# Kernel optimization log

Measured on AMD Instinct MI355X. Metric: run time of the kernel, lower is better.

## Reference

```python
import jax, jax.numpy as jnp
import numpy as np

SCALE_MIN, SCALE_MAX = 0.01, 10.0
LN_EPS = 1e-5

B, KIN, H, C = 32, 6144, 512, 5


def _kaiming_uniform(k, shape):
    # torch kaiming_uniform_(a=sqrt(5)) on (out,in): bound = 1/sqrt(fan_in)
    bound = 1.0 / np.sqrt(shape[1])
    return jax.random.uniform(k, shape, minval=-bound, maxval=bound, dtype=jnp.float32)


def setup_inputs() -> dict:
    key = jax.random.key(0)
    ks = jax.random.split(key, 16)
    inp = {"x": jax.random.normal(ks[0], (B, KIN), dtype=jnp.float32)}
    dims = [(H, KIN), (H, H), (H, H)]
    for i, (o, n) in enumerate(dims):
        inp[f"w{i}"] = _kaiming_uniform(ks[1 + 3 * i], (o, n))
        inp[f"t{i}"] = jax.random.uniform(ks[2 + 3 * i], (o, n), minval=-1.0, maxval=1.0, dtype=jnp.float32)
        inp[f"s{i}"] = jax.random.uniform(ks[3 + 3 * i], (o, n), minval=-2.0, maxval=0.0, dtype=jnp.float32)
        inp[f"g{i}"] = jnp.ones((o,), jnp.float32)
        inp[f"b{i}"] = jnp.zeros((o,), jnp.float32)
    inp["cw"] = _kaiming_uniform(ks[10], (C, H))
    cbound = 1.0 / np.sqrt(H)
    inp["cb"] = jax.random.uniform(ks[11], (C,), minval=-cbound, maxval=cbound, dtype=jnp.float32)
    return inp


def _wavelet_linear(h, w, t, sr):
    # h: (B, in), params: (out, in)
    scale = SCALE_MIN + (SCALE_MAX - SCALE_MIN) * jax.nn.sigmoid(sr)
    s = (h[:, None, :] - t[None]) / (scale[None] + 1e-8)  # (B, out, in)
    psi = (1.0 - s * s) * jnp.exp(-0.5 * s * s)  # mexican hat
    return jnp.einsum('boi,oi->bo', psi, w)


def _layer_norm(h, g, b):
    m = jnp.mean(h, axis=-1, keepdims=True)
    v = jnp.mean(jnp.square(h - m), axis=-1, keepdims=True)
    return (h - m) * jax.lax.rsqrt(v + LN_EPS) * g + b


def reference(x, w0, t0, s0, g0, b0, w1, t1, s1, g1, b1, w2, t2, s2, g2, b2, cw, cb):
    h = x
    for (w, t, sr, g, b) in [(w0, t0, s0, g0, b0), (w1, t1, s1, g1, b1), (w2, t2, s2, g2, b2)]:
        h = _layer_norm(jax.nn.silu(_wavelet_linear(h, w, t, sr)), g, b)
    return h @ cw.T + cb
```

## Files before the change

### kernel.cpp

```cpp
#include <hip/hip_runtime.h>

#define LN_EPS 1e-5f
#define LOG2E 1.44269504f
#define NHALF_LOG2E (-0.72134752f)

#if __has_builtin(__builtin_amdgcn_exp2f)
#define EXP2F(x) __builtin_amdgcn_exp2f(x)
#else
#define EXP2F(x) __expf((x) * 0.69314718f)
#endif


constexpr int NBLK   = 512;
constexpr int TPB    = 512;
constexpr int NWAVES = NBLK * (TPB / 64);
constexpr int NGRP   = 16;
constexpr int GRP    = NBLK / NGRP;
constexpr int PADX   = 34;

__device__ __forceinline__ float sysld(const float* p)
{
    return __hip_atomic_load(p, __ATOMIC_RELAXED, __HIP_MEMORY_SCOPE_SYSTEM);
}
__device__ __forceinline__ void sysst(float* p, float v)
{
    __hip_atomic_store(p, v, __ATOMIC_RELAXED, __HIP_MEMORY_SCOPE_SYSTEM);
}
__device__ __forceinline__ float2 sysld2(const float* p)
{
    unsigned long long v = __hip_atomic_load((const unsigned long long*)p,
        __ATOMIC_RELAXED, __HIP_MEMORY_SCOPE_SYSTEM);
    union { unsigned long long u; float2 f; } c; c.u = v; return c.f;
}
__device__ __forceinline__ void sysst2(float* p, float a, float b)
{
    union { unsigned long long u; float2 f; } c; c.f = make_float2(a, b);
    __hip_atomic_store((unsigned long long*)p, c.u, __ATOMIC_RELAXED,
                       __HIP_MEMORY_SCOPE_SYSTEM);
}

__device__ __forceinline__ void gridbar(int* __restrict__ bar, int k)
{
    asm volatile("s_waitcnt vmcnt(0)" ::: "memory");
    __syncthreads();
    if (threadIdx.x == 0) {
        const int g = blockIdx.x >> 5;
        int* grpArr = bar + g * 32;
        int* grpRel = bar + (NGRP + g) * 32;
        int* gArr   = bar + 2 * NGRP * 32;

        int old = __hip_atomic_fetch_add(grpArr, 1, __ATOMIC_RELAXED,
                                         __HIP_MEMORY_SCOPE_AGENT);
        if (old == k * GRP - 1) {
            int o2 = __hip_atomic_fetch_add(gArr, 1, __ATOMIC_RELAXED,
                                            __HIP_MEMORY_SCOPE_AGENT);
            if (o2 == k * NGRP - 1) {
#pragma unroll
                for (int j = 0; j < NGRP; ++j)
                    __hip_atomic_store(bar + (NGRP + j) * 32, k,
                                       __ATOMIC_RELAXED, __HIP_MEMORY_SCOPE_AGENT);
            }
        }
        while (__hip_atomic_load(grpRel, __ATOMIC_RELAXED,
                                 __HIP_MEMORY_SCOPE_AGENT) < k)
            __builtin_amdgcn_s_sleep(8);
    }
    __syncthreads();
}

__device__ __forceinline__ void wav0_phase(const float* __restrict__ x,
        const float* __restrict__ w, const float* __restrict__ t,
        const float* __restrict__ s, float* __restrict__ part,
        float4* __restrict__ myPrep, float* __restrict__ xs,
        int lane, int wave)
{
    constexpr int RANGE = 192, STEPS = RANGE / 4, TPW = 4;
    const int si    = blockIdx.x >> 4;
    const int obase = (blockIdx.x & 15) * 32;
    const int ibase = si * RANGE;

    for (int b = wave; b < 32; b += 8)
        for (int i2 = lane; i2 < RANGE; i2 += 64)
            xs[i2 * PADX + b] = x[b * 6144 + ibase + i2];
    __syncthreads();

    const int p = lane & 15, g = lane >> 4;
    const int o0 = obase + wave * TPW;
    const float* __restrict__ wp = w + (size_t)o0 * 6144 + ibase;
    const float* __restrict__ tp = t + (size_t)o0 * 6144 + ibase;
    const float* __restrict__ sp = s + (size_t)o0 * 6144 + ibase;

    float fw[3], ft[3], fs[3];
#pragma unroll
    for (int r = 0; r < 3; ++r) {
        int il = r * 64 + lane;
        fw[r] = wp[il]; ft[r] = tp[il]; fs[r] = sp[il];
    }

#pragma unroll
    for (int ti = 0; ti < TPW; ++ti) {
#pragma unroll
        for (int r = 0; r < 3; ++r) {
            int il = r * 64 + lane;
            float sig = __builtin_amdgcn_rcpf(1.f + EXP2F(-fs[r] * LOG2E));
            float inv = __builtin_amdgcn_rcpf(fmaf(9.99f, sig, 0.01000001f));
            myPrep[il] = make_float4(inv, -ft[r] * inv, fw[r], 0.f);
        }
        if (ti + 1 < TPW) {
            const float* wpn = wp + (size_t)(ti + 1) * 6144;
            const float* tpn = tp + (size_t)(ti + 1) * 6144;
            const float* spn = sp + (size_t)(ti + 1) * 6144;
#pragma unroll
            for (int r = 0; r < 3; ++r) {
                int il = r * 64 + lane;
                fw[r] = wpn[il]; ft[r] = tpn[il]; fs[r] = spn[il];
            }
        }

        float acc0 = 0.f, acc1 = 0.f;
#pragma unroll 8
        for (int st = 0; st < STEPS; ++st) {
            float4 pr = myPrep[st * 4 + g];
            float2 xv = *(const float2*)&xs[(st * 4 + g) * PADX + 2 * p];
            float u0 = fmaf(xv.x, pr.x, pr.y);
            float u1 = fmaf(xv.y, pr.x, pr.y);
            float q0 = u0 * u0, q1 = u1 * u1;
            float e0 = EXP2F(q0 * NHALF_LOG2E);
            float e1 = EXP2F(q1 * NHALF_LOG2E);
            float pw0 = fmaf(-pr.z, q0, pr.z);
            float pw1 = fmaf(-pr.z, q1, pr.z);
            acc0 = fmaf(pw0, e0, acc0);
            acc1 = fmaf(pw1, e1, acc1);
        }

        acc0 += __shfl_down(acc0, 32); acc0 += __shfl_down(acc0, 16);
        acc1 += __shfl_down(acc1, 32); acc1 += __shfl_down(acc1, 16);
        if (lane < 16) {
            const int o = o0 + ti;
            sysst2(part + (size_t)si * 16384 + o * 32 + 2 * p, acc0, acc1);
        }
    }
}

__device__ __forceinline__ void wav12_phase(const float* __restrict__ hin,
        float* __restrict__ part, float4* __restrict__ myPrep,
        int lane, int gw, float fw, float ft, float fs)
{
    constexpr int STEPS = 16;
    const int p = lane & 15, g = lane >> 4;
    const int o = gw & 511, si = gw >> 9;
    const int ibase = si * 64;

    {
        float sig = __builtin_amdgcn_rcpf(1.f + EXP2F(-fs * LOG2E));
        float inv = __builtin_amdgcn_rcpf(fmaf(9.99f, sig, 0.01000001f));
        myPrep[lane] = make_float4(inv, -ft * inv, fw, 0.f);
    }

    const float* __restrict__ hp = hin + (size_t)(ibase + g) * 32 + 2 * p;

    float acc0 = 0.f, acc1 = 0.f;
#pragma unroll 8
    for (int st = 0; st < STEPS; ++st) {
        float4 pr = myPrep[st * 4 + g];
        float2 xv = sysld2(hp + (size_t)st * 128);
        float u0 = fmaf(xv.x, pr.x, pr.y);
        float u1 = fmaf(xv.y, pr.x, pr.y);
        float q0 = u0 * u0, q1 = u1 * u1;
        float e0 = EXP2F(q0 * NHALF_LOG2E);
        float e1 = EXP2F(q1 * NHALF_LOG2E);
        float pw0 = fmaf(-pr.z, q0, pr.z);
        float pw1 = fmaf(-pr.z, q1, pr.z);
        acc0 = fmaf(pw0, e0, acc0);
        acc1 = fmaf(pw1, e1, acc1);
    }

    acc0 += __shfl_down(acc0, 32); acc0 += __shfl_down(acc0, 16);
    acc1 += __shfl_down(acc1, 32); acc1 += __shfl_down(acc1, 16);
    if (lane < 16)
        sysst2(part + (size_t)si * 16384 + o * 32 + 2 * p, acc0, acc1);
}

template<int S>
__device__ __forceinline__ void ln_phase(const float* __restrict__ part,
        const float* __restrict__ gam, const float* __restrict__ bet,
        float* __restrict__ hT, float* __restrict__ r1, float* __restrict__ r2)
{
    if (blockIdx.x < 32) {
        const int b = blockIdx.x, tid = threadIdx.x;
        float v = 0.f;
#pragma unroll
        for (int si = 0; si < S; ++si)
            v += sysld(part + (size_t)si * 16384 + tid * 32 + b);
        float a = v * __builtin_amdgcn_rcpf(1.f + EXP2F(-v * LOG2E));

        float s1 = a, s2 = a * a;
#pragma unroll
        for (int off = 32; off; off >>= 1) {
            s1 += __shfl_down(s1, off);
            s2 += __shfl_down(s2, off);
        }
        const int lane = tid & 63, wid = tid >> 6;
        if (lane == 0) { r1[wid] = s1; r2[wid] = s2; }
        __syncthreads();
        float t1 = 0.f, t2 = 0.f;
#pragma unroll
        for (int k = 0; k < 8; ++k) { t1 += r1[k]; t2 += r2[k]; }
        float m   = t1 * (1.f / 512.f);
        float var = t2 * (1.f / 512.f) - m * m;
        float r   = __builtin_amdgcn_rsqf(var + LN_EPS);
        sysst(hT + tid * 32 + b, (a - m) * r * gam[tid] + bet[tid]);
    }
}

template<int S>
__device__ __forceinline__ void cls_phase(const float* __restrict__ part,
        const float* __restrict__ gam, const float* __restrict__ bet,
        const float* __restrict__ cw, const float* __restrict__ cb,
        float* __restrict__ out, float* __restrict__ r1, float* __restrict__ r2,
        float (* __restrict__ cr)[8])
{
    if (blockIdx.x < 32) {
        const int b = blockIdx.x, tid = threadIdx.x;
        float v = 0.f;
#pragma unroll
        for (int si = 0; si < S; ++si)
            v += sysld(part + (size_t)si * 16384 + tid * 32 + b);
        float a = v * __builtin_amdgcn_rcpf(1.f + EXP2F(-v * LOG2E));

        float s1 = a, s2 = a * a;
#pragma unroll
        for (int off = 32; off; off >>= 1) {
            s1 += __shfl_down(s1, off);
            s2 += __shfl_down(s2, off);
        }
        const int lane = tid & 63, wid = tid >> 6;
        if (lane == 0) { r1[wid] = s1; r2[wid] = s2; }
        __syncthreads();
        float t1 = 0.f, t2 = 0.f;
#pragma unroll
        for (int k = 0; k < 8; ++k) { t1 += r1[k]; t2 += r2[k]; }
        float m   = t1 * (1.f / 512.f);
        float var = t2 * (1.f / 512.f) - m * m;
        float r   = __builtin_amdgcn_rsqf(var + LN_EPS);
        float hl  = (a - m) * r * gam[tid] + bet[tid];

#pragma unroll
        for (int c = 0; c < 5; ++c) {
            float pv = hl * cw[c * 512 + tid];
#pragma unroll
            for (int off = 32; off; off >>= 1) pv += __shfl_down(pv, off);
            if (lane == 0) cr[c][wid] = pv;
        }
        __syncthreads();
        if (tid < 5) {
            float sum = 0.f;
#pragma unroll
            for (int k = 0; k < 8; ++k) sum += cr[tid][k];
            out[b * 5 + tid] = sum + cb[tid];
        }
    }
}

__global__ __launch_bounds__(TPB, 4)
void megakernel(const float* __restrict__ x,
                const float* __restrict__ w0, const float* __restrict__ t0,
                const float* __restrict__ s0, const float* __restrict__ g0,
                const float* __restrict__ b0,
                const float* __restrict__ w1, const float* __restrict__ t1,
                const float* __restrict__ s1, const float* __restrict__ g1,
                const float* __restrict__ b1,
                const float* __restrict__ w2, const float* __restrict__ t2,
                const float* __restrict__ s2, const float* __restrict__ g2,
                const float* __restrict__ b2,
                const float* __restrict__ cw, const float* __restrict__ cb,
                float* __restrict__ out,
                float* __restrict__ part, float* __restrict__ hT,
                int* __restrict__ bar)
{
    __shared__ float4 prep[8][192];
    __shared__ float  xs[192 * PADX];
    __shared__ float  r1[8], r2[8], cr[5][8];

    const int wave = threadIdx.x >> 6, lane = threadIdx.x & 63;
    const int gw = blockIdx.x * (TPB / 64) + wave;
    float4* myPrep = prep[wave];

    wav0_phase(x, w0, t0, s0, part, myPrep, xs, lane, wave);
    const int o1 = gw & 511, si1 = gw >> 9;
    const size_t off1 = (size_t)o1 * 512 + si1 * 64 + lane;
    float fw1 = w1[off1], ft1 = t1[off1], fs1 = s1[off1];
    gridbar(bar, 1);
    ln_phase<32>(part, g0, b0, hT, r1, r2);
    gridbar(bar, 2);

    wav12_phase(hT, part, myPrep, lane, gw, fw1, ft1, fs1);
    float fw2 = w2[off1], ft2 = t2[off1], fs2 = s2[off1];
    gridbar(bar, 3);
    ln_phase<8>(part, g1, b1, hT, r1, r2);
    gridbar(bar, 4);

    wav12_phase(hT, part, myPrep, lane, gw, fw2, ft2, fs2);
    gridbar(bar, 5);
    cls_phase<8>(part, g2, b2, cw, cb, out, r1, r2, cr);
}

extern "C" void kernel_launch(void* const* d_in, const int* in_sizes, int n_in,
                              void* d_out, int out_size, void* d_ws, size_t ws_size,
                              hipStream_t stream)
{
    const float* x  = (const float*)d_in[0];
    const float* w0 = (const float*)d_in[1];
    const float* t0 = (const float*)d_in[2];
    const float* s0 = (const float*)d_in[3];
    const float* g0 = (const float*)d_in[4];
    const float* b0 = (const float*)d_in[5];
    const float* w1 = (const float*)d_in[6];
    const float* t1 = (const float*)d_in[7];
    const float* s1 = (const float*)d_in[8];
    const float* g1 = (const float*)d_in[9];
    const float* b1 = (const float*)d_in[10];
    const float* w2 = (const float*)d_in[11];
    const float* t2 = (const float*)d_in[12];
    const float* s2 = (const float*)d_in[13];
    const float* g2 = (const float*)d_in[14];
    const float* b2 = (const float*)d_in[15];
    const float* cw = (const float*)d_in[16];
    const float* cb = (const float*)d_in[17];
    float* out = (float*)d_out;

    float* part = (float*)d_ws;
    float* hT   = part + 32 * 16384;
    int*   bar  = (int*)(hT + 16384);

    hipMemsetAsync(bar, 0, 8192, stream);

    void* args[] = { (void*)&x,
                     (void*)&w0, (void*)&t0, (void*)&s0, (void*)&g0, (void*)&b0,
                     (void*)&w1, (void*)&t1, (void*)&s1, (void*)&g1, (void*)&b1,
                     (void*)&w2, (void*)&t2, (void*)&s2, (void*)&g2, (void*)&b2,
                     (void*)&cw, (void*)&cb, (void*)&out,
                     (void*)&part, (void*)&hT, (void*)&bar };

    hipLaunchKernel((const void*)megakernel, dim3(NBLK), dim3(TPB),
                    args, 0, stream);
}
```

Measured before the change: 179.2 us.

## Replace split-K partial buffers with atomic accumulation and redundant per-block LayerNorm

Split-K partial sums are now accumulated directly into zeroed (batch, out) buffers with float atomicAdd, instead of being written to per-slice partial arrays and reduced later. Every block then redundantly reads the full accumulated layer output and computes SiLU and LayerNorm statistics itself, keeping its 64-row input slice in LDS. This removes the separate LN phase and two of the five grid barriers. The cost is redundant global reads and reductions in all 512 blocks, atomic contention on the accumulators, a larger memset, and a summation order that is no longer deterministic.

```diff
diff --git a/kernel.cpp b/kernel.cpp
--- a/kernel.cpp
+++ b/kernel.cpp
@@ -13,30 +13,14 @@
 
 constexpr int NBLK   = 512;
 constexpr int TPB    = 512;
-constexpr int NWAVES = NBLK * (TPB / 64);
 constexpr int NGRP   = 16;
 constexpr int GRP    = NBLK / NGRP;
 constexpr int PADX   = 34;
+constexpr int PADH   = 33;
 
 __device__ __forceinline__ float sysld(const float* p)
 {
     return __hip_atomic_load(p, __ATOMIC_RELAXED, __HIP_MEMORY_SCOPE_SYSTEM);
-}
-__device__ __forceinline__ void sysst(float* p, float v)
-{
-    __hip_atomic_store(p, v, __ATOMIC_RELAXED, __HIP_MEMORY_SCOPE_SYSTEM);
-}
-__device__ __forceinline__ float2 sysld2(const float* p)
-{
-    unsigned long long v = __hip_atomic_load((const unsigned long long*)p,
-        __ATOMIC_RELAXED, __HIP_MEMORY_SCOPE_SYSTEM);
-    union { unsigned long long u; float2 f; } c; c.u = v; return c.f;
-}
-__device__ __forceinline__ void sysst2(float* p, float a, float b)
-{
-    union { unsigned long long u; float2 f; } c; c.f = make_float2(a, b);
-    __hip_atomic_store((unsigned long long*)p, c.u, __ATOMIC_RELAXED,
-                       __HIP_MEMORY_SCOPE_SYSTEM);
 }
 
 __device__ __forceinline__ void gridbar(int* __restrict__ bar, int k)
@@ -68,9 +52,23 @@
     __syncthreads();
 }
 
+__device__ __forceinline__ void acc_atomic(float* __restrict__ hacc, int o,
+                                           float acc0, float acc1, int lane)
+{
+    acc0 += __shfl_down(acc0, 32); acc0 += __shfl_down(acc0, 16);
+    acc1 += __shfl_down(acc1, 32); acc1 += __shfl_down(acc1, 16);
+    int srcl = (lane < 16) ? lane : (lane - 16);
+    float a1 = __shfl(acc1, srcl);
+    if (lane < 32) {
+        int   b  = (lane < 16) ? (lane << 1) : (((lane - 16) << 1) | 1);
+        float av = (lane < 16) ? acc0 : a1;
+        atomicAdd(hacc + (size_t)b * 512 + o, av);
+    }
+}
+
 __device__ __forceinline__ void wav0_phase(const float* __restrict__ x,
         const float* __restrict__ w, const float* __restrict__ t,
-        const float* __restrict__ s, float* __restrict__ part,
+        const float* __restrict__ s, float* __restrict__ hacc,
         float4* __restrict__ myPrep, float* __restrict__ xs,
         int lane, int wave)
 {
@@ -132,24 +130,57 @@
             acc0 = fmaf(pw0, e0, acc0);
             acc1 = fmaf(pw1, e1, acc1);
         }
-
-        acc0 += __shfl_down(acc0, 32); acc0 += __shfl_down(acc0, 16);
-        acc1 += __shfl_down(acc1, 32); acc1 += __shfl_down(acc1, 16);
-        if (lane < 16) {
-            const int o = o0 + ti;
-            sysst2(part + (size_t)si * 16384 + o * 32 + 2 * p, acc0, acc1);
-        }
-    }
-}
-
-__device__ __forceinline__ void wav12_phase(const float* __restrict__ hin,
-        float* __restrict__ part, float4* __restrict__ myPrep,
+        acc_atomic(hacc, o0 + ti, acc0, acc1, lane);
+    }
+}
+
+__device__ __forceinline__ void ln_red(const float* __restrict__ hacc,
+        const float* __restrict__ gam, const float* __restrict__ bet,
+        float* __restrict__ h_lds, float (* __restrict__ redS)[32],
+        float (* __restrict__ redQ)[32], int si_blk)
+{
+    const int t = threadIdx.x, lane = t & 63, wid = t >> 6;
+    float a[32];
+#pragma unroll
+    for (int b = 0; b < 32; ++b) {
+        float v = sysld(hacc + (size_t)b * 512 + t);
+        a[b] = v * __builtin_amdgcn_rcpf(1.f + EXP2F(-v * LOG2E));
+    }
+#pragma unroll
+    for (int b = 0; b < 32; ++b) {
+        float u = a[b], q = a[b] * a[b];
+#pragma unroll
+        for (int off = 32; off; off >>= 1) {
+            u += __shfl_xor(u, off);
+            q += __shfl_xor(q, off);
+        }
+        if (lane == 0) { redS[wid][b] = u; redQ[wid][b] = q; }
+    }
+    __syncthreads();
+    if (wid == si_blk) {
+        const int row = lane;
+        float gm = gam[t], bt = bet[t];
+#pragma unroll
+        for (int b = 0; b < 32; ++b) {
+            float t1 = 0.f, t2 = 0.f;
+#pragma unroll
+            for (int w2 = 0; w2 < 8; ++w2) { t1 += redS[w2][b]; t2 += redQ[w2][b]; }
+            float m   = t1 * (1.f / 512.f);
+            float var = t2 * (1.f / 512.f) - m * m;
+            float r   = __builtin_amdgcn_rsqf(var + LN_EPS);
+            h_lds[row * PADH + b] = (a[b] - m) * r * gm + bt;
+        }
+    }
+    __syncthreads();
+}
+
+__device__ __forceinline__ void wav12_phase(const float* __restrict__ h_lds,
+        float* __restrict__ hacc, float4* __restrict__ myPrep,
         int lane, int gw, float fw, float ft, float fs)
 {
     constexpr int STEPS = 16;
     const int p = lane & 15, g = lane >> 4;
-    const int o = gw & 511, si = gw >> 9;
-    const int ibase = si * 64;
+    const int o = gw & 511;
 
     {
         float sig = __builtin_amdgcn_rcpf(1.f + EXP2F(-fs * LOG2E));
@@ -157,15 +188,15 @@
         myPrep[lane] = make_float4(inv, -ft * inv, fw, 0.f);
     }
 
-    const float* __restrict__ hp = hin + (size_t)(ibase + g) * 32 + 2 * p;
-
     float acc0 = 0.f, acc1 = 0.f;
 #pragma unroll 8
     for (int st = 0; st < STEPS; ++st) {
         float4 pr = myPrep[st * 4 + g];
-        float2 xv = sysld2(hp + (size_t)st * 128);
-        float u0 = fmaf(xv.x, pr.x, pr.y);
-        float u1 = fmaf(xv.y, pr.x, pr.y);
+        int row = g + 4 * st;
+        float x0 = h_lds[row * PADH + 2 * p];
+        float x1 = h_lds[row * PADH + 2 * p + 1];
+        float u0 = fmaf(x0, pr.x, pr.y);
+        float u1 = fmaf(x1, pr.x, pr.y);
         float q0 = u0 * u0, q1 = u1 * u1;
         float e0 = EXP2F(q0 * NHALF_LOG2E);
         float e1 = EXP2F(q1 * NHALF_LOG2E);
@@ -174,47 +205,10 @@
         acc0 = fmaf(pw0, e0, acc0);
         acc1 = fmaf(pw1, e1, acc1);
     }
-
-    acc0 += __shfl_down(acc0, 32); acc0 += __shfl_down(acc0, 16);
-    acc1 += __shfl_down(acc1, 32); acc1 += __shfl_down(acc1, 16);
-    if (lane < 16)
-        sysst2(part + (size_t)si * 16384 + o * 32 + 2 * p, acc0, acc1);
-}
-
-template<int S>
-__device__ __forceinline__ void ln_phase(const float* __restrict__ part,
-        const float* __restrict__ gam, const float* __restrict__ bet,
-        float* __restrict__ hT, float* __restrict__ r1, float* __restrict__ r2)
-{
-    if (blockIdx.x < 32) {
-        const int b = blockIdx.x, tid = threadIdx.x;
-        float v = 0.f;
-#pragma unroll
-        for (int si = 0; si < S; ++si)
-            v += sysld(part + (size_t)si * 16384 + tid * 32 + b);
-        float a = v * __builtin_amdgcn_rcpf(1.f + EXP2F(-v * LOG2E));
-
-        float s1 = a, s2 = a * a;
-#pragma unroll
-        for (int off = 32; off; off >>= 1) {
-            s1 += __shfl_down(s1, off);
-            s2 += __shfl_down(s2, off);
-        }
-        const int lane = tid & 63, wid = tid >> 6;
-        if (lane == 0) { r1[wid] = s1; r2[wid] = s2; }
-        __syncthreads();
-        float t1 = 0.f, t2 = 0.f;
-#pragma unroll
-        for (int k = 0; k < 8; ++k) { t1 += r1[k]; t2 += r2[k]; }
-        float m   = t1 * (1.f / 512.f);
-        float var = t2 * (1.f / 512.f) - m * m;
-        float r   = __builtin_amdgcn_rsqf(var + LN_EPS);
-        sysst(hT + tid * 32 + b, (a - m) * r * gam[tid] + bet[tid]);
-    }
-}
-
-template<int S>
-__device__ __forceinline__ void cls_phase(const float* __restrict__ part,
+    acc_atomic(hacc, o, acc0, acc1, lane);
+}
+
+__device__ __forceinline__ void cls_phase(const float* __restrict__ hacc,
         const float* __restrict__ gam, const float* __restrict__ bet,
         const float* __restrict__ cw, const float* __restrict__ cb,
         float* __restrict__ out, float* __restrict__ r1, float* __restrict__ r2,
@@ -222,10 +216,7 @@
 {
     if (blockIdx.x < 32) {
         const int b = blockIdx.x, tid = threadIdx.x;
-        float v = 0.f;
-#pragma unroll
-        for (int si = 0; si < S; ++si)
-            v += sysld(part + (size_t)si * 16384 + tid * 32 + b);
+        float v = sysld(hacc + (size_t)b * 512 + tid);
         float a = v * __builtin_amdgcn_rcpf(1.f + EXP2F(-v * LOG2E));
 
         float s1 = a, s2 = a * a;
@@ -275,34 +266,36 @@
                 const float* __restrict__ b2,
                 const float* __restrict__ cw, const float* __restrict__ cb,
                 float* __restrict__ out,
-                float* __restrict__ part, float* __restrict__ hT,
-                int* __restrict__ bar)
+                float* __restrict__ hacc0, float* __restrict__ hacc1,
+                float* __restrict__ hacc2, int* __restrict__ bar)
 {
     __shared__ float4 prep[8][192];
     __shared__ float  xs[192 * PADX];
+    __shared__ float  h_lds[64 * PADH];
+    __shared__ float  redS[8][32], redQ[8][32];
     __shared__ float  r1[8], r2[8], cr[5][8];
 
     const int wave = threadIdx.x >> 6, lane = threadIdx.x & 63;
     const int gw = blockIdx.x * (TPB / 64) + wave;
+    const int si_blk = blockIdx.x >> 6;
     float4* myPrep = prep[wave];
 
-    wav0_phase(x, w0, t0, s0, part, myPrep, xs, lane, wave);
-    const int o1 = gw & 511, si1 = gw >> 9;
-    const size_t off1 = (size_t)o1 * 512 + si1 * 64 + lane;
+    wav0_phase(x, w0, t0, s0, hacc0, myPrep, xs, lane, wave);
+    const int o1 = gw & 511;
+    const size_t off1 = (size_t)o1 * 512 + si_blk * 64 + lane;
     float fw1 = w1[off1], ft1 = t1[off1], fs1 = s1[off1];
     gridbar(bar, 1);
-    ln_phase<32>(part, g0, b0, hT, r1, r2);
+
+    ln_red(hacc0, g0, b0, h_lds, redS, redQ, si_blk);
+    wav12_phase(h_lds, hacc1, myPrep, lane, gw, fw1, ft1, fs1);
+    float fw2 = w2[off1], ft2 = t2[off1], fs2 = s2[off1];
     gridbar(bar, 2);
 
-    wav12_phase(hT, part, myPrep, lane, gw, fw1, ft1, fs1);
-    float fw2 = w2[off1], ft2 = t2[off1], fs2 = s2[off1];
+    ln_red(hacc1, g1, b1, h_lds, redS, redQ, si_blk);
+    wav12_phase(h_lds, hacc2, myPrep, lane, gw, fw2, ft2, fs2);
     gridbar(bar, 3);
-    ln_phase<8>(part, g1, b1, hT, r1, r2);
-    gridbar(bar, 4);
-
-    wav12_phase(hT, part, myPrep, lane, gw, fw2, ft2, fs2);
-    gridbar(bar, 5);
-    cls_phase<8>(part, g2, b2, cw, cb, out, r1, r2, cr);
+
+    cls_phase(hacc2, g2, b2, cw, cb, out, r1, r2, cr);
 }
 
 extern "C" void kernel_launch(void* const* d_in, const int* in_sizes, int n_in,
@@ -329,18 +322,19 @@
     const float* cb = (const float*)d_in[17];
     float* out = (float*)d_out;
 
-    float* part = (float*)d_ws;
-    float* hT   = part + 32 * 16384;
-    int*   bar  = (int*)(hT + 16384);
-
-    hipMemsetAsync(bar, 0, 8192, stream);
+    float* hacc0 = (float*)d_ws;
+    float* hacc1 = hacc0 + 16384;
+    float* hacc2 = hacc1 + 16384;
+    int*   bar   = (int*)(hacc2 + 16384);
+
+    hipMemsetAsync(d_ws, 0, 3 * 16384 * 4 + 8192, stream);
 
     void* args[] = { (void*)&x,
                      (void*)&w0, (void*)&t0, (void*)&s0, (void*)&g0, (void*)&b0,
                      (void*)&w1, (void*)&t1, (void*)&s1, (void*)&g1, (void*)&b1,
                      (void*)&w2, (void*)&t2, (void*)&s2, (void*)&g2, (void*)&b2,
                      (void*)&cw, (void*)&cb, (void*)&out,
-                     (void*)&part, (void*)&hT, (void*)&bar };
+                     (void*)&hacc0, (void*)&hacc1, (void*)&hacc2, (void*)&bar };
 
     hipLaunchKernel((const void*)megakernel, dim3(NBLK), dim3(TPB),
                     args, 0, stream);
```

Measured after the change: 202.1 us. +12.8%, slower.
